# Kernel optimization log

Hardware: AMD Instinct MI355X
Metric: run time of the kernel (lower is better)

Reference implementation:

```python
import jax, jax.numpy as jnp
import numpy as np
from jax import lax

B, CIN, H, W = 32, 128, 64, 64
COUT, K, NK, HID = 128, 3, 4, 32
TEMP = 34.0
PAD = 1


def setup_inputs() -> dict:
    key = jax.random.key(0)
    k1, k2, k3, k4 = jax.random.split(key, 4)
    x = jax.random.normal(k1, (B, CIN, H, W), dtype=jnp.float32)
    fc1_w = jax.random.normal(k2, (HID, CIN), dtype=jnp.float32) * (2.0 / CIN) ** 0.5
    fc2_w = jax.random.normal(k3, (NK, HID), dtype=jnp.float32) * (2.0 / HID) ** 0.5
    fc2_b = jnp.zeros((NK,), dtype=jnp.float32)
    weight = jax.random.normal(k4, (NK, COUT, CIN, K, K), dtype=jnp.float32) * 0.05
    bias = jnp.zeros((NK, COUT), dtype=jnp.float32)
    return {"x": x, "fc1_w": fc1_w, "fc2_w": fc2_w, "fc2_b": fc2_b,
            "weight": weight, "bias": bias}


def _per_sample_conv(xi, wi):
    # xi: [CIN, H, W], wi: [COUT, CIN, K, K]
    out = lax.conv_general_dilated(
        xi[None], wi,
        window_strides=(1, 1),
        padding=[(PAD, PAD), (PAD, PAD)],
        dimension_numbers=("NCHW", "OIHW", "NCHW"))
    return out[0]  # [COUT, H', W']


def reference(x, fc1_w, fc2_w, fc2_b, weight, bias):
    # attention: global avg pool -> 1x1 conv (matmul) -> relu -> 1x1 conv -> softmax
    context = jnp.mean(x, axis=(2, 3))                      # [B, CIN]
    hid = jax.nn.relu(context @ fc1_w.T)                    # [B, HID]
    logits = hid @ fc2_w.T + fc2_b                          # [B, NK]
    att = jax.nn.softmax(logits / TEMP, axis=1)             # [B, NK]
    # aggregate per-sample kernels and biases
    agg_w = jnp.einsum("bk,koihw->boihw", att, weight)      # [B, COUT, CIN, K, K]
    agg_b = att @ bias                                      # [B, COUT]
    # per-sample convolution (equivalent to the groups=B trick in torch)
    out = jax.vmap(_per_sample_conv)(x, agg_w)              # [B, COUT, H, W]
    return out + agg_b[:, :, None, None]
```

## Files before the change

### kernel.cpp

```cpp
#include <hip/hip_runtime.h>

#define B_    32
#define CIN_  128
#define H_    64
#define W_    64
#define COUT_ 128
#define NK_   4
#define HID_  32
#define TEMP_ 34.0f

typedef short bf16x8 __attribute__((ext_vector_type(8)));
typedef float f32x16 __attribute__((ext_vector_type(16)));

__device__ __forceinline__ short f2bf(float f) {
    union { float f; unsigned u; } c; c.f = f;
    unsigned r = (c.u + 0x7FFFu + ((c.u >> 16) & 1u)) >> 16;
    return (short)r;
}

__global__ __launch_bounds__(256) void k_context(const float* __restrict__ x,
                                                 float* __restrict__ ctx) {
    const int row = blockIdx.x * 4 + (threadIdx.x >> 6);
    const int lane = threadIdx.x & 63;
    const float* p = x + (size_t)row * (H_ * W_);
    float s = 0.f;
#pragma unroll
    for (int k = 0; k < 16; ++k) {
        float4 v = *(const float4*)(p + lane * 4 + k * 256);
        s += v.x + v.y + v.z + v.w;
    }
    for (int off = 32; off > 0; off >>= 1) s += __shfl_down(s, off, 64);
    if (lane == 0) ctx[row] = s * (1.0f / (H_ * W_));
}

__global__ __launch_bounds__(256) void k_aggw(const float* __restrict__ ctx,
        const float* __restrict__ fc1w, const float* __restrict__ fc2w,
        const float* __restrict__ fc2b, const float* __restrict__ bias,
        const float* __restrict__ weight, short* __restrict__ aggwt,
        float* __restrict__ aggb) {
    __shared__ float hidp[8][32];
    __shared__ float shid[32];
    __shared__ float satt[NK_];
    __shared__ float sbuf[2 * 128 * 17];
    const int t = threadIdx.x;
    const int blk = blockIdx.x;
    const int b = blk >> 6;
    const int co0 = (blk & 63) * 2;
    {
        const int hh = t & 31, part = t >> 5;
        const float* c  = ctx + b * CIN_ + part * 16;
        const float* f1 = fc1w + hh * CIN_ + part * 16;
        float s = 0.f;
#pragma unroll
        for (int j = 0; j < 16; ++j) s += c[j] * f1[j];
        hidp[part][hh] = s;
    }
    __syncthreads();
    if (t < 32) {
        float s = 0.f;
#pragma unroll
        for (int p = 0; p < 8; ++p) s += hidp[p][t];
        shid[t] = fmaxf(s, 0.f);
    }
    __syncthreads();
    if (t == 0) {
        float lg[NK_]; float mx = -1e30f;
#pragma unroll
        for (int k = 0; k < NK_; ++k) {
            float s = fc2b[k];
            for (int hh = 0; hh < HID_; ++hh) s += shid[hh] * fc2w[k * HID_ + hh];
            lg[k] = s / TEMP_; mx = fmaxf(mx, lg[k]);
        }
        float den = 0.f;
#pragma unroll
        for (int k = 0; k < NK_; ++k) { lg[k] = expf(lg[k] - mx); den += lg[k]; }
        const float rd = 1.0f / den;
#pragma unroll
        for (int k = 0; k < NK_; ++k) satt[k] = lg[k] * rd;
    }
    __syncthreads();
    const float a0 = satt[0], a1 = satt[1], a2 = satt[2], a3 = satt[3];

    if ((t & 127) == 0) {
        const int co = co0 + (t >> 7);
        aggb[b * COUT_ + co] = a0 * bias[co] + a1 * bias[COUT_ + co]
                             + a2 * bias[2 * COUT_ + co] + a3 * bias[3 * COUT_ + co];
    }

    const size_t kstride = (size_t)COUT_ * CIN_ * 9;
    const float* W0 = weight + (size_t)co0 * (CIN_ * 9);
#pragma unroll
    for (int jj = 0; jj < 3; ++jj) {
        const int i4 = jj * 256 + t;
        if (i4 < 576) {
            const float4 w0 = *(const float4*)(W0 + i4 * 4);
            const float4 w1 = *(const float4*)(W0 + kstride + i4 * 4);
            const float4 w2 = *(const float4*)(W0 + 2 * kstride + i4 * 4);
            const float4 w3 = *(const float4*)(W0 + 3 * kstride + i4 * 4);
            float r4[4];
            r4[0] = a0 * w0.x + a1 * w1.x + a2 * w2.x + a3 * w3.x;
            r4[1] = a0 * w0.y + a1 * w1.y + a2 * w2.y + a3 * w3.y;
            r4[2] = a0 * w0.z + a1 * w1.z + a2 * w2.z + a3 * w3.z;
            r4[3] = a0 * w0.w + a1 * w1.w + a2 * w2.w + a3 * w3.w;
#pragma unroll
            for (int j = 0; j < 4; ++j) {
                const unsigned f = (unsigned)(i4 * 4 + j);
                const unsigned ci = f / 9u;
                const unsigned rr = f - ci * 9u;
                sbuf[ci * 17 + rr] = r4[j];
            }
        }
    }
    __syncthreads();
#pragma unroll
    for (int jj = 0; jj < 2; ++jj) {
        const int g = jj * 256 + t;
        if (g < 288) {
            const int coL = (g >= 144) ? 1 : 0;
            const int gg = g - coL * 144;
            const int r  = gg >> 4;
            const int oc = gg & 15;
            const int co = co0 + coL;
            const float* src = &sbuf[(coL * 128 + oc * 8) * 17 + r];
            bf16x8 v;
#pragma unroll
            for (int e = 0; e < 8; ++e)
                v[e] = f2bf(src[e * 17]);
            short* dst = aggwt
                + ((size_t)(((b * 4 + (co >> 5)) * 9 + r) * 8 + (oc >> 1)) * 512)
                + ((co & 31) * 2 + (oc & 1)) * 8;
            *(bf16x8*)dst = v;
        }
    }
}

#define RBY 8448
#define RSH 4224
__global__ __launch_bounds__(256, 2) void k_conv(const float* __restrict__ x,
        const short* __restrict__ aggwt, const float* __restrict__ aggb,
        float* __restrict__ out) {
    __shared__ short xt[6 * RSH];
    const int tid = threadIdx.x;
    const int blk = blockIdx.x;
    const int b = blk & 31;
    const int h0 = (blk >> 5) * 4;
    const int lane = tid & 63;
    const int wv = tid >> 6;
    const int l31 = lane & 31;
    const int lane5 = lane >> 5;

    if (tid < 96) {
        const int row = tid >> 4;
        const int q = tid & 15;
        const int cl = (q < 8) ? q : (512 + q);
        *(int4*)(&xt[row * RSH + cl * 8]) = make_int4(0, 0, 0, 0);
    }

    f32x16 acc[8];
#pragma unroll
    for (int t = 0; t < 8; ++t)
#pragma unroll
        for (int k = 0; k < 16; ++k) acc[t][k] = 0.f;

    const short* Ap = aggwt + (size_t)(b * 4 + wv) * (9 * 8 * 512)
                            + (size_t)(l31 * 2 + lane5) * 8;

#pragma unroll
    for (int k = 0; k < 12; ++k) {
        const int task = k * 4 + wv;
        const int row = task >> 3;
        const int g = task & 7;
        const int in_h = h0 - 1 + row;
        bf16x8 v = (bf16x8){0, 0, 0, 0, 0, 0, 0, 0};
        if (in_h >= 0 && in_h < H_) {
            const float* gp = x + (((size_t)b * CIN_ + g * 8) * H_ + in_h) * W_ + lane;
            float f[8];
#pragma unroll
            for (int j = 0; j < 8; ++j) f[j] = gp[j * (H_ * W_)];
#pragma unroll
            for (int j = 0; j < 8; ++j) v[j] = f2bf(f[j]);
        }
        *(bf16x8*)(&xt[row * RSH + ((lane + 1) * 8 + ((g + lane) & 7)) * 8]) = v;
    }
    __syncthreads();

#pragma unroll
    for (int kc = 0; kc < 8; ++kc) {
        float sf[3][8];
        if (kc < 4) {
#pragma unroll
            for (int k = 0; k < 3; ++k) {
                const int task = k * 4 + wv;
                const int row = task >> 1;
                const int j = task & 1;
                const int in_h = h0 - 1 + row;
                if (in_h >= 0 && in_h < H_) {
                    const float* gp = x + (((size_t)b * CIN_ + 64 + (2 * kc + j) * 8) * H_
                                           + in_h) * W_ + lane;
#pragma unroll
                    for (int jj = 0; jj < 8; ++jj) sf[k][jj] = gp[jj * (H_ * W_)];
                }
            }
        }
        bf16x8 av[9];
#pragma unroll
        for (int r = 0; r < 9; ++r)
            av[r] = *(const bf16x8*)(Ap + ((size_t)(r * 8 + kc)) * 512);
        const int kcl = kc & 3;
        __builtin_amdgcn_s_setprio(1);
#pragma unroll
        for (int ir = 0; ir < 6; ++ir) {
            bf16x8 bv[2][3];
#pragma unroll
            for (int i = 0; i < 2; ++i)
#pragma unroll
                for (int kw = 0; kw < 3; ++kw) {
                    const int s = i * 32 + l31 + kw;
                    const int off = 16 * ((2 * kcl + lane5 + s - 1) & 7);
                    bv[i][kw] = *(const bf16x8*)((const char*)xt + ir * RBY + s * 128 + off);
                }
#pragma unroll
            for (int orr = 0; orr < 4; ++orr) {
                if (orr <= ir && ir <= orr + 2) {
                    const int kh = ir - orr;
#pragma unroll
                    for (int i = 0; i < 2; ++i)
#pragma unroll
                        for (int kw = 0; kw < 3; ++kw)
                            acc[orr * 2 + i] = __builtin_amdgcn_mfma_f32_32x32x16_bf16(
                                av[kh * 3 + kw], bv[i][kw], acc[orr * 2 + i], 0, 0, 0);
                }
            }
        }
        __builtin_amdgcn_s_setprio(0);
        if (kc <= 4) __syncthreads();
        if (kc < 4) {
#pragma unroll
            for (int k = 0; k < 3; ++k) {
                const int task = k * 4 + wv;
                const int row = task >> 1;
                const int j = task & 1;
                const int in_h = h0 - 1 + row;
                const int g = 2 * kc + j;
                bf16x8 v = (bf16x8){0, 0, 0, 0, 0, 0, 0, 0};
                if (in_h >= 0 && in_h < H_) {
#pragma unroll
                    for (int jj = 0; jj < 8; ++jj) v[jj] = f2bf(sf[k][jj]);
                }
                *(bf16x8*)(&xt[row * RSH + ((lane + 1) * 8 + ((g + lane) & 7)) * 8]) = v;
            }
        }
    }

    const float* ab = aggb + b * COUT_;
#pragma unroll
    for (int orr = 0; orr < 4; ++orr) {
#pragma unroll
        for (int i = 0; i < 2; ++i) {
            const int hh = h0 + orr;
            const int w = i * 32 + l31;
            float* op = out + ((size_t)b * COUT_ * H_ + hh) * W_ + w;
            const f32x16 a = acc[orr * 2 + i];
#pragma unroll
            for (int reg = 0; reg < 16; ++reg) {
                const int co = wv * 32 + (reg & 3) + 8 * (reg >> 2) + 4 * lane5;
                op[(size_t)co * (H_ * W_)] = a[reg] + ab[co];
            }
        }
    }
}

extern "C" void kernel_launch(void* const* d_in, const int* in_sizes, int n_in,
                              void* d_out, int out_size, void* d_ws, size_t ws_size,
                              hipStream_t stream) {
    const float* x    = (const float*)d_in[0];
    const float* fc1w = (const float*)d_in[1];
    const float* fc2w = (const float*)d_in[2];
    const float* fc2b = (const float*)d_in[3];
    const float* wgt  = (const float*)d_in[4];
    const float* bias = (const float*)d_in[5];
    float* out = (float*)d_out;

    char* ws = (char*)d_ws;
    float* ctx   = (float*)(ws + 0);
    float* aggb  = (float*)(ws + 16384);
    short* aggwt = (short*)(ws + 65536);

    k_context<<<dim3(B_ * CIN_ / 4), dim3(256), 0, stream>>>(x, ctx);
    k_aggw<<<dim3(B_ * (COUT_ / 2)), dim3(256), 0, stream>>>(
        ctx, fc1w, fc2w, fc2b, bias, wgt, aggwt, aggb);
    k_conv<<<dim3(B_ * (H_ / 4)), dim3(256), 0, stream>>>(x, aggwt, aggb, out);
}
```

Baseline: 162.0 us.

## Split conv tiles along width to halve per-block work and raise occupancy

Each conv block now covers 32 output columns instead of 64, doubling the grid to 1024 blocks. Accumulators drop from 8 to 4 tiles and shared memory roughly halves, so launch bounds are raised to allow 3 blocks per CU. The input staging loads a 34-column halo window with explicit boundary zeroing. The trade-off is that the weight fragments per block are now loaded twice as often and the halo columns add extra input loads.

```diff
diff --git a/kernel.cpp b/kernel.cpp
--- a/kernel.cpp
+++ b/kernel.cpp
@@ -134,31 +134,27 @@
     }
 }
 
-#define RBY 8448
-#define RSH 4224
-__global__ __launch_bounds__(256, 2) void k_conv(const float* __restrict__ x,
+#define RBY2 4352
+#define RSH2 2176
+__global__ __launch_bounds__(256, 3) void k_conv(const float* __restrict__ x,
         const short* __restrict__ aggwt, const float* __restrict__ aggb,
         float* __restrict__ out) {
-    __shared__ short xt[6 * RSH];
+    __shared__ short xt[6 * RSH2];
     const int tid = threadIdx.x;
     const int blk = blockIdx.x;
     const int b = blk & 31;
-    const int h0 = (blk >> 5) * 4;
+    const int rest = blk >> 5;
+    const int h0 = (rest >> 1) * 4;
+    const int iw = rest & 1;
     const int lane = tid & 63;
     const int wv = tid >> 6;
     const int l31 = lane & 31;
     const int lane5 = lane >> 5;
-
-    if (tid < 96) {
-        const int row = tid >> 4;
-        const int q = tid & 15;
-        const int cl = (q < 8) ? q : (512 + q);
-        *(int4*)(&xt[row * RSH + cl * 8]) = make_int4(0, 0, 0, 0);
-    }
-
-    f32x16 acc[8];
-#pragma unroll
-    for (int t = 0; t < 8; ++t)
+    const int wslot = iw * 32 - 1 + lane;
+
+    f32x16 acc[4];
+#pragma unroll
+    for (int t = 0; t < 4; ++t)
 #pragma unroll
         for (int k = 0; k < 16; ++k) acc[t][k] = 0.f;
 
@@ -171,16 +167,18 @@
         const int row = task >> 3;
         const int g = task & 7;
         const int in_h = h0 - 1 + row;
-        bf16x8 v = (bf16x8){0, 0, 0, 0, 0, 0, 0, 0};
-        if (in_h >= 0 && in_h < H_) {
-            const float* gp = x + (((size_t)b * CIN_ + g * 8) * H_ + in_h) * W_ + lane;
-            float f[8];
-#pragma unroll
-            for (int j = 0; j < 8; ++j) f[j] = gp[j * (H_ * W_)];
-#pragma unroll
-            for (int j = 0; j < 8; ++j) v[j] = f2bf(f[j]);
-        }
-        *(bf16x8*)(&xt[row * RSH + ((lane + 1) * 8 + ((g + lane) & 7)) * 8]) = v;
+        if (lane < 34) {
+            bf16x8 v = (bf16x8){0, 0, 0, 0, 0, 0, 0, 0};
+            if (in_h >= 0 && in_h < H_ && wslot >= 0 && wslot < W_) {
+                const float* gp = x + (((size_t)b * CIN_ + g * 8) * H_ + in_h) * W_ + wslot;
+                float f[8];
+#pragma unroll
+                for (int j = 0; j < 8; ++j) f[j] = gp[j * (H_ * W_)];
+#pragma unroll
+                for (int j = 0; j < 8; ++j) v[j] = f2bf(f[j]);
+            }
+            *(bf16x8*)(&xt[row * RSH2 + lane * 64 + ((g + lane - 1) & 7) * 8]) = v;
+        }
     }
     __syncthreads();
 
@@ -194,9 +192,9 @@
                 const int row = task >> 1;
                 const int j = task & 1;
                 const int in_h = h0 - 1 + row;
-                if (in_h >= 0 && in_h < H_) {
+                if (lane < 34 && in_h >= 0 && in_h < H_ && wslot >= 0 && wslot < W_) {
                     const float* gp = x + (((size_t)b * CIN_ + 64 + (2 * kc + j) * 8) * H_
-                                           + in_h) * W_ + lane;
+                                           + in_h) * W_ + wslot;
 #pragma unroll
                     for (int jj = 0; jj < 8; ++jj) sf[k][jj] = gp[jj * (H_ * W_)];
                 }
@@ -210,25 +208,21 @@
         __builtin_amdgcn_s_setprio(1);
 #pragma unroll
         for (int ir = 0; ir < 6; ++ir) {
-            bf16x8 bv[2][3];
-#pragma unroll
-            for (int i = 0; i < 2; ++i)
-#pragma unroll
-                for (int kw = 0; kw < 3; ++kw) {
-                    const int s = i * 32 + l31 + kw;
-                    const int off = 16 * ((2 * kcl + lane5 + s - 1) & 7);
-                    bv[i][kw] = *(const bf16x8*)((const char*)xt + ir * RBY + s * 128 + off);
-                }
+            bf16x8 bv[3];
+#pragma unroll
+            for (int kw = 0; kw < 3; ++kw) {
+                const int s = l31 + kw;
+                const int off = 16 * ((2 * kcl + lane5 + s - 1) & 7);
+                bv[kw] = *(const bf16x8*)((const char*)xt + ir * RBY2 + s * 128 + off);
+            }
 #pragma unroll
             for (int orr = 0; orr < 4; ++orr) {
                 if (orr <= ir && ir <= orr + 2) {
                     const int kh = ir - orr;
 #pragma unroll
-                    for (int i = 0; i < 2; ++i)
-#pragma unroll
-                        for (int kw = 0; kw < 3; ++kw)
-                            acc[orr * 2 + i] = __builtin_amdgcn_mfma_f32_32x32x16_bf16(
-                                av[kh * 3 + kw], bv[i][kw], acc[orr * 2 + i], 0, 0, 0);
+                    for (int kw = 0; kw < 3; ++kw)
+                        acc[orr] = __builtin_amdgcn_mfma_f32_32x32x16_bf16(
+                            av[kh * 3 + kw], bv[kw], acc[orr], 0, 0, 0);
                 }
             }
         }
@@ -242,12 +236,14 @@
                 const int j = task & 1;
                 const int in_h = h0 - 1 + row;
                 const int g = 2 * kc + j;
-                bf16x8 v = (bf16x8){0, 0, 0, 0, 0, 0, 0, 0};
-                if (in_h >= 0 && in_h < H_) {
-#pragma unroll
-                    for (int jj = 0; jj < 8; ++jj) v[jj] = f2bf(sf[k][jj]);
+                if (lane < 34) {
+                    bf16x8 v = (bf16x8){0, 0, 0, 0, 0, 0, 0, 0};
+                    if (in_h >= 0 && in_h < H_ && wslot >= 0 && wslot < W_) {
+#pragma unroll
+                        for (int jj = 0; jj < 8; ++jj) v[jj] = f2bf(sf[k][jj]);
+                    }
+                    *(bf16x8*)(&xt[row * RSH2 + lane * 64 + ((g + lane - 1) & 7) * 8]) = v;
                 }
-                *(bf16x8*)(&xt[row * RSH + ((lane + 1) * 8 + ((g + lane) & 7)) * 8]) = v;
             }
         }
     }
@@ -255,17 +251,14 @@
     const float* ab = aggb + b * COUT_;
 #pragma unroll
     for (int orr = 0; orr < 4; ++orr) {
-#pragma unroll
-        for (int i = 0; i < 2; ++i) {
-            const int hh = h0 + orr;
-            const int w = i * 32 + l31;
-            float* op = out + ((size_t)b * COUT_ * H_ + hh) * W_ + w;
-            const f32x16 a = acc[orr * 2 + i];
-#pragma unroll
-            for (int reg = 0; reg < 16; ++reg) {
-                const int co = wv * 32 + (reg & 3) + 8 * (reg >> 2) + 4 * lane5;
-                op[(size_t)co * (H_ * W_)] = a[reg] + ab[co];
-            }
+        const int hh = h0 + orr;
+        const int w = iw * 32 + l31;
+        float* op = out + ((size_t)b * COUT_ * H_ + hh) * W_ + w;
+        const f32x16 a = acc[orr];
+#pragma unroll
+        for (int reg = 0; reg < 16; ++reg) {
+            const int co = wv * 32 + (reg & 3) + 8 * (reg >> 2) + 4 * lane5;
+            op[(size_t)co * (H_ * W_)] = a[reg] + ab[co];
         }
     }
 }
@@ -289,5 +282,5 @@
     k_context<<<dim3(B_ * CIN_ / 4), dim3(256), 0, stream>>>(x, ctx);
     k_aggw<<<dim3(B_ * (COUT_ / 2)), dim3(256), 0, stream>>>(
         ctx, fc1w, fc2w, fc2b, bias, wgt, aggwt, aggb);
-    k_conv<<<dim3(B_ * (H_ / 4)), dim3(256), 0, stream>>>(x, aggwt, aggb, out);
-}
+    k_conv<<<dim3(B_ * (H_ / 4) * 2), dim3(256), 0, stream>>>(x, aggwt, aggb, out);
+}
```

New measurement: 170.4 us. 1.05x slower.
